# Performance work log

Hardware: AMD Instinct MI355X
Metric: run time of the kernel (lower is better)

## Reference

```python
import math
import jax, jax.numpy as jnp
import numpy as np

B = 4096
IN_FEATURES = 512
OUT_FEATURES = 1024
SPARSITY = 0.01  # kwta.sparsity
X_DENSITY = 0.1  # fraction of active bits in the binary SDR input


def setup_inputs() -> dict:
    key = jax.random.key(0)
    kx, kw = jax.random.split(key)
    # binary sparse SDR input (the module counts nonzeros, expects sparse binary x)
    x = (jax.random.uniform(kx, (B, IN_FEATURES)) < X_DENSITY).astype(jnp.float32)
    weight = jax.random.normal(kw, (OUT_FEATURES, IN_FEATURES), dtype=jnp.float32)
    return {"x": x, "weight": weight}


def reference(x, weight):
    Bn, in_f = x.shape
    out_f = weight.shape[0]
    k_active = math.ceil(SPARSITY * out_f)   # serial MP steps (11)
    k_in = math.ceil(SPARSITY * in_f)        # kwta winners on xr (6)
    rows = jnp.arange(Bn)

    nonzero = jnp.sum(x != 0, axis=1)
    lambd = (3 * jnp.max(nonzero) * in_f).astype(jnp.float32)

    def wta(r):  # one-hot argmax per row -> binary [B, out_f]
        idx = jnp.argmax(r, axis=1)
        return jnp.zeros_like(r).at[rows, idx].set(1.0)

    def kwta(v):  # binary top-k per row -> binary [B, in_f]
        _, idx = jax.lax.top_k(v, k_in)
        return jnp.zeros_like(v).at[rows[:, None], idx].set(1.0)

    two_x = 2.0 * x
    wT = weight.T  # [in_f, out_f]

    def step(carry, _):
        encoded, xr = carry
        residual = (two_x - xr) @ wT - lambd * encoded      # [B, out_f]
        encoded = encoded + wta(residual)
        xr = kwta(encoded @ weight)                          # [B, in_f]
        return (encoded, xr), None

    init = (jnp.zeros((Bn, out_f), jnp.float32), jnp.zeros_like(x))
    (encoded, xr), _ = jax.lax.scan(step, init, None, length=k_active)
    return encoded, xr
```

## Files before the change

kernel.cpp:

```cpp
#include <hip/hip_runtime.h>

#define IN_F 512
#define OUT_F 1024
#define K_ACTIVE 11
#define K_IN 6

__global__ __launch_bounds__(256) void transpose_w_kernel(const float* __restrict__ w,
                                                          float* __restrict__ wT) {
    __shared__ float tile[32][33];
    const int tx = threadIdx.x & 31;
    const int ty = threadIdx.x >> 5;
    const int i0 = blockIdx.x * 32;
    const int j0 = blockIdx.y * 32;
#pragma unroll
    for (int k = 0; k < 4; ++k)
        tile[ty + 8 * k][tx] = w[(size_t)(j0 + ty + 8 * k) * IN_F + (i0 + tx)];
    __syncthreads();
#pragma unroll
    for (int k = 0; k < 4; ++k)
        wT[(size_t)(i0 + ty + 8 * k) * OUT_F + (j0 + tx)] = tile[tx][ty + 8 * k];
}
__global__ void zero_row_f_kernel(float* __restrict__ wT) {
    wT[(size_t)IN_F * OUT_F + blockIdx.x * 256 + threadIdx.x] = 0.0f;
}

__device__ __forceinline__ unsigned long long pack_key(double v, unsigned rev,
                                                       unsigned long long mask) {
    unsigned long long b = (unsigned long long)__double_as_longlong(v);
    unsigned long long m =
        (unsigned long long)((long long)b >> 63) | 0x8000000000000000ull;
    unsigned long long u = b ^ m;
    return (u & ~mask) | (unsigned long long)rev;
}

__device__ __forceinline__ unsigned hi_key(double v) {
    const int hi = __double2hiint(v);
    return (unsigned)hi ^ ((unsigned)(hi >> 31) | 0x80000000u);
}

template <int C>
__device__ __forceinline__ unsigned maxdpp(unsigned v) {
    unsigned t = (unsigned)__builtin_amdgcn_update_dpp(0, (int)v, C, 0xF, 0xF, true);
    return t > v ? t : v;
}
__device__ __forceinline__ unsigned wave_umax(unsigned v) {
    v = maxdpp<0x111>(v);
    v = maxdpp<0x112>(v);
    v = maxdpp<0x114>(v);
    v = maxdpp<0x118>(v);
    v = maxdpp<0x142>(v);
    v = maxdpp<0x143>(v);
    return (unsigned)__builtin_amdgcn_readlane((int)v, 63);
}

__device__ __forceinline__ unsigned long long wave_max_key(unsigned long long k) {
    const unsigned h = (unsigned)(k >> 32), l = (unsigned)k;
    const unsigned gh = wave_umax(h);
    const unsigned long long tied = __ballot(h == gh);
    unsigned gl;
    if (__popcll(tied) == 1) {
        gl = (unsigned)__builtin_amdgcn_readlane((int)l,
                                                 (int)__ffsll((long long)tied) - 1);
    } else {
        gl = wave_umax((h == gh) ? l : 0u);
    }
    return ((unsigned long long)gh << 32) | gl;
}

__device__ __forceinline__ void half_add2(double* rh, const float* __restrict__ wT,
                                          int i0, int i1, int lane, int wv) {
    const float* p0 = wT + ((size_t)i0 << 10) + (wv << 9) + (lane << 2);
    const float* p1 = wT + ((size_t)i1 << 10) + (wv << 9) + (lane << 2);
    const float4 f0 = *(const float4*)(p0);
    const float4 f1 = *(const float4*)(p0 + 256);
    const float4 g0 = *(const float4*)(p1);
    const float4 g1 = *(const float4*)(p1 + 256);
    rh[0] += (double)f0.x + (double)g0.x;  rh[1] += (double)f0.y + (double)g0.y;
    rh[2] += (double)f0.z + (double)g0.z;  rh[3] += (double)f0.w + (double)g0.w;
    rh[4] += (double)f1.x + (double)g1.x;  rh[5] += (double)f1.y + (double)g1.y;
    rh[6] += (double)f1.z + (double)g1.z;  rh[7] += (double)f1.w + (double)g1.w;
}

__device__ __forceinline__ void half_axpy(double* rh, const float* __restrict__ wT,
                                          int i, double sgn, int lane, int wv) {
    const float* rp = wT + ((size_t)i << 10) + (wv << 9) + (lane << 2);
    const float4 f0 = *(const float4*)(rp);
    const float4 f1 = *(const float4*)(rp + 256);
    rh[0] += sgn * (double)f0.x;  rh[1] += sgn * (double)f0.y;
    rh[2] += sgn * (double)f0.z;  rh[3] += sgn * (double)f0.w;
    rh[4] += sgn * (double)f1.x;  rh[5] += sgn * (double)f1.y;
    rh[6] += sgn * (double)f1.z;  rh[7] += sgn * (double)f1.w;
}

__device__ __forceinline__ void half_add0(double* rh, const float* __restrict__ w,
                                          int i, int lane, int wv) {
#pragma unroll
    for (int s = 0; s < 8; ++s) {
        const int j = (wv << 9) | ((s >> 2) << 8) | (lane << 2) | (s & 3);
        rh[s] += (double)w[(size_t)j * IN_F + i];
    }
}
__device__ __forceinline__ void half_axpy0(double* rh, const float* __restrict__ w,
                                           int i, double sgn, int lane, int wv) {
#pragma unroll
    for (int s = 0; s < 8; ++s) {
        const int j = (wv << 9) | ((s >> 2) << 8) | (lane << 2) | (s & 3);
        rh[s] += sgn * (double)w[(size_t)j * IN_F + i];
    }
}

template <int MODE>
__global__ __launch_bounds__(128) void bmp_kernel(const float* __restrict__ x,
                                                  const float* __restrict__ w,
                                                  const float* __restrict__ wT,
                                                  float* __restrict__ out, int rows) {
    __shared__ unsigned short act[IN_F + 8];
    __shared__ unsigned gu32[2][2];
    __shared__ int gjw[2][2];
    __shared__ unsigned long long kx[2];
    const int lane = threadIdx.x & 63;
    const int wv = threadIdx.x >> 6;
    const int row = blockIdx.x;
    if (row >= rows) return;

    const float* xrow = x + (size_t)row * IN_F;
    int cnt = 0;
#pragma unroll
    for (int c = 0; c < IN_F / 64; ++c) {
        bool pbit = xrow[c * 64 + lane] != 0.0f;
        unsigned long long m = __ballot(pbit);
        int pre = __popcll(m & ((1ull << lane) - 1ull));
        if (wv == 0 && pbit) act[cnt + pre] = (unsigned short)(c * 64 + lane);
        cnt += __popcll(m);
    }
    if (wv == 0 && lane < 2) act[cnt + lane] = (unsigned short)IN_F;
    __syncthreads();

    double r[8];
#pragma unroll
    for (int s = 0; s < 8; ++s) r[s] = 0.0;
    if constexpr (MODE == 1) {
#pragma unroll 1
        for (int k = 0; k < cnt; k += 2) half_add2(r, wT, act[k], act[k + 1], lane, wv);
    } else {
#pragma unroll 1
        for (int k = 0; k < cnt; ++k) half_add0(r, w, act[k], lane, wv);
    }
#pragma unroll
    for (int s = 0; s < 8; ++s) r[s] *= 2.0;

    double vd[8];
#pragma unroll
    for (int p = 0; p < 8; ++p) vd[p] = 0.0;

    unsigned enc = 0;
    unsigned selmask = 0;
    int O0 = -1, O1 = -1, O2 = -1, O3 = -1, O4 = -1, O5 = -1;

#pragma unroll 1
    for (int t = 0; t < K_ACTIVE; ++t) {
        unsigned k8[8];
#pragma unroll
        for (int s = 0; s < 8; ++s) {
            const unsigned key = hi_key(r[s]);
            k8[s] = (enc & (1u << s)) ? 0u : key;
        }
        {
            unsigned lm = k8[0];
#pragma unroll
            for (int s = 1; s < 8; ++s) lm = k8[s] > lm ? k8[s] : lm;
            const unsigned g = wave_umax(lm);
            const unsigned long long tied = __ballot(lm == g);
            unsigned mm = 0;
#pragma unroll
            for (int s = 0; s < 8; ++s) mm |= (k8[s] == g) ? (1u << s) : 0u;
            const int L = (int)__ffsll((long long)tied) - 1;
            const unsigned mmL = (unsigned)__builtin_amdgcn_readlane((int)mm, L);
            int jw;
            if (__builtin_expect((__popcll(tied) == 1) && !(mmL & (mmL - 1)), 1)) {
                const int bi = __ffs(mmL) - 1;
                jw = (wv << 9) | ((bi >> 2) << 8) | (L << 2) | (bi & 3);
            } else {
                unsigned long long kb = 0;
#pragma unroll
                for (int s = 0; s < 8; ++s) {
                    const int j = (wv << 9) | ((s >> 2) << 8) | (lane << 2) | (s & 3);
                    const unsigned long long fk =
                        pack_key(r[s], 1023u ^ (unsigned)j, 1023ull);
                    kb = (k8[s] == g && fk > kb) ? fk : kb;
                }
                const unsigned long long gk = wave_max_key(kb);
                jw = 1023 ^ (int)(gk & 1023ull);
            }
            if (lane == 0) {
                gu32[t & 1][wv] = g;
                gjw[t & 1][wv] = jw;
            }
        }
        __syncthreads();
        const unsigned ga = gu32[t & 1][0], gb = gu32[t & 1][1];
        int bestj;
        if (__builtin_expect(ga != gb, 1)) {
            bestj = (gb > ga) ? gjw[t & 1][1] : gjw[t & 1][0];
        } else {
            unsigned long long kb = 0;
#pragma unroll
            for (int s = 0; s < 8; ++s) {
                const int j = (wv << 9) | ((s >> 2) << 8) | (lane << 2) | (s & 3);
                const unsigned long long fk =
                    pack_key(r[s], 1023u ^ (unsigned)j, 1023ull);
                kb = (k8[s] == ga && fk > kb) ? fk : kb;
            }
            const unsigned long long wm = wave_max_key(kb);
            if (lane == 0) kx[wv] = wm;
            __syncthreads();
            const unsigned long long A = kx[0], B = kx[1];
            bestj = 1023 ^ (int)((A > B ? A : B) & 1023ull);
        }
        bestj = __builtin_amdgcn_readfirstlane(bestj);
        if ((bestj >> 9) == wv && ((bestj >> 2) & 63) == lane)
            enc |= 1u << ((((bestj >> 8) & 1) << 2) | (bestj & 3));

        {
            const float* wr = w + ((size_t)bestj << 9) + (lane << 2);
            const float4 f0 = *(const float4*)wr;
            const float4 f1 = *(const float4*)(wr + 256);
            vd[0] += (double)f0.x;  vd[1] += (double)f0.y;
            vd[2] += (double)f0.z;  vd[3] += (double)f0.w;
            vd[4] += (double)f1.x;  vd[5] += (double)f1.y;
            vd[6] += (double)f1.z;  vd[7] += (double)f1.w;
        }

        int N0, N1, N2, N3, N4, N5;
        {
            unsigned kk[8];
#pragma unroll
            for (int p = 0; p < 8; ++p) kk[p] = hi_key(vd[p]);
            int N[6];
#pragma unroll
            for (int s2 = 0; s2 < K_IN; ++s2) {
                unsigned lm = kk[0];
#pragma unroll
                for (int p = 1; p < 8; ++p) lm = kk[p] > lm ? kk[p] : lm;
                const unsigned g2 = wave_umax(lm);
                const unsigned long long tied2 = __ballot(lm == g2);
                unsigned mm2 = 0;
#pragma unroll
                for (int p = 0; p < 8; ++p) mm2 |= (kk[p] == g2) ? (1u << p) : 0u;
                const int L2 = (int)__ffsll((long long)tied2) - 1;
                const unsigned mmL2 =
                    (unsigned)__builtin_amdgcn_readlane((int)mm2, L2);
                int n;
                if (__builtin_expect((__popcll(tied2) == 1) && !(mmL2 & (mmL2 - 1)),
                                     1)) {
                    const int bp = __ffs(mmL2) - 1;
                    n = ((bp >> 2) << 8) | (L2 << 2) | (bp & 3);
#pragma unroll
                    for (int p = 0; p < 8; ++p) kk[p] = (kk[p] == g2) ? 0u : kk[p];
                } else {
                    unsigned long long kb = 0;
#pragma unroll
                    for (int p = 0; p < 8; ++p) {
                        const int i = ((p >> 2) << 8) | (lane << 2) | (p & 3);
                        const unsigned long long fk =
                            pack_key(vd[p], 511u ^ (unsigned)i, 511ull);
                        kb = (kk[p] == g2 && fk > kb) ? fk : kb;
                    }
                    const unsigned long long gk = wave_max_key(kb);
                    n = 511 ^ (int)(gk & 511ull);
                    const int ln = (n >> 2) & 63;
                    const int bp = (((n >> 8) & 1) << 2) | (n & 3);
#pragma unroll
                    for (int p = 0; p < 8; ++p)
                        kk[p] = (lane == ln && p == bp) ? 0u : kk[p];
                }
                N[s2] = __builtin_amdgcn_readfirstlane(n);
            }
            if (t == K_ACTIVE - 1) {
                selmask = 0;
#pragma unroll
                for (int p = 0; p < 8; ++p) selmask |= (kk[p] == 0u) ? (1u << p) : 0u;
            }
            N0 = N[0]; N1 = N[1]; N2 = N[2]; N3 = N[3]; N4 = N[4]; N5 = N[5];
        }

        if (t == 0) {
            if constexpr (MODE == 1) {
                half_axpy(r, wT, N0, -1.0, lane, wv);
                half_axpy(r, wT, N1, -1.0, lane, wv);
                half_axpy(r, wT, N2, -1.0, lane, wv);
                half_axpy(r, wT, N3, -1.0, lane, wv);
                half_axpy(r, wT, N4, -1.0, lane, wv);
                half_axpy(r, wT, N5, -1.0, lane, wv);
            } else {
                half_axpy0(r, w, N0, -1.0, lane, wv);
                half_axpy0(r, w, N1, -1.0, lane, wv);
                half_axpy0(r, w, N2, -1.0, lane, wv);
                half_axpy0(r, w, N3, -1.0, lane, wv);
                half_axpy0(r, w, N4, -1.0, lane, wv);
                half_axpy0(r, w, N5, -1.0, lane, wv);
            }
        } else if (t < K_ACTIVE - 1) {
#pragma unroll
            for (int a2 = 0; a2 < 6; ++a2) {
                const int o = (a2 == 0) ? O0 : (a2 == 1) ? O1 : (a2 == 2) ? O2
                              : (a2 == 3) ? O3 : (a2 == 4) ? O4 : O5;
                const bool stay = (o == N0) | (o == N1) | (o == N2) |
                                  (o == N3) | (o == N4) | (o == N5);
                if (!stay) {
                    if constexpr (MODE == 1) half_axpy(r, wT, o, 1.0, lane, wv);
                    else half_axpy0(r, w, o, 1.0, lane, wv);
                }
            }
#pragma unroll
            for (int b2 = 0; b2 < 6; ++b2) {
                const int n = (b2 == 0) ? N0 : (b2 == 1) ? N1 : (b2 == 2) ? N2
                              : (b2 == 3) ? N3 : (b2 == 4) ? N4 : N5;
                const bool was = (n == O0) | (n == O1) | (n == O2) |
                                 (n == O3) | (n == O4) | (n == O5);
                if (!was) {
                    if constexpr (MODE == 1) half_axpy(r, wT, n, -1.0, lane, wv);
                    else half_axpy0(r, w, n, -1.0, lane, wv);
                }
            }
        }
        O0 = N0; O1 = N1; O2 = N2; O3 = N3; O4 = N4; O5 = N5;
    }

    float* oe = out + (size_t)row * OUT_F + (wv << 9) + (lane << 2);
#pragma unroll
    for (int c = 0; c < 2; ++c) {
        float4 v;
        v.x = (enc & (1u << (4 * c + 0))) ? 1.0f : 0.0f;
        v.y = (enc & (1u << (4 * c + 1))) ? 1.0f : 0.0f;
        v.z = (enc & (1u << (4 * c + 2))) ? 1.0f : 0.0f;
        v.w = (enc & (1u << (4 * c + 3))) ? 1.0f : 0.0f;
        *(float4*)(oe + (c << 8)) = v;
    }
    if (wv == 0) {
        float* ox = out + (size_t)rows * OUT_F + (size_t)row * IN_F + (lane << 2);
#pragma unroll
        for (int c = 0; c < 2; ++c) {
            float4 v;
            v.x = (selmask & (1u << (4 * c + 0))) ? 1.0f : 0.0f;
            v.y = (selmask & (1u << (4 * c + 1))) ? 1.0f : 0.0f;
            v.z = (selmask & (1u << (4 * c + 2))) ? 1.0f : 0.0f;
            v.w = (selmask & (1u << (4 * c + 3))) ? 1.0f : 0.0f;
            *(float4*)(ox + (c << 8)) = v;
        }
    }
}

extern "C" void kernel_launch(void* const* d_in, const int* in_sizes, int n_in,
                              void* d_out, int out_size, void* d_ws, size_t ws_size,
                              hipStream_t stream) {
    const float* x = (const float*)d_in[0];
    const float* w = (const float*)d_in[1];
    float* out = (float*)d_out;
    const int rows = in_sizes[0] / IN_F;

    const size_t need_f = (size_t)(IN_F + 1) * OUT_F * sizeof(float);

    if (d_ws != nullptr && ws_size >= need_f) {
        float* wT = (float*)d_ws;
        transpose_w_kernel<<<dim3(IN_F / 32, OUT_F / 32), 256, 0, stream>>>(w, wT);
        zero_row_f_kernel<<<OUT_F / 256, 256, 0, stream>>>(wT);
        bmp_kernel<1><<<rows, 128, 0, stream>>>(x, w, wT, out, rows);
    } else {
        bmp_kernel<0><<<rows, 128, 0, stream>>>(x, w, nullptr, out, rows);
    }
}
```

Measured before the change: 156.2 us.

## Process two rows per block, splitting the kWTA stage across waves

Result: slower. 196.5 us (+25.8%).

```diff
diff --git a/kernel.cpp b/kernel.cpp
--- a/kernel.cpp
+++ b/kernel.cpp
@@ -110,98 +110,91 @@
 }
 
 template <int MODE>
-__global__ __launch_bounds__(128) void bmp_kernel(const float* __restrict__ x,
-                                                  const float* __restrict__ w,
-                                                  const float* __restrict__ wT,
-                                                  float* __restrict__ out, int rows) {
-    __shared__ unsigned short act[IN_F + 8];
+__global__ __launch_bounds__(128, 4) void bmp_kernel(const float* __restrict__ x,
+                                                     const float* __restrict__ w,
+                                                     const float* __restrict__ wT,
+                                                     float* __restrict__ out,
+                                                     int rows) {
+    __shared__ unsigned short act[2][IN_F + 8];
+    __shared__ int cntS[2];
     __shared__ unsigned gu32[2][2];
     __shared__ int gjw[2][2];
-    __shared__ unsigned long long kx[2];
+    __shared__ unsigned long long kx[2][2];
+    __shared__ int msg[2][8];
     const int lane = threadIdx.x & 63;
     const int wv = threadIdx.x >> 6;
-    const int row = blockIdx.x;
-    if (row >= rows) return;
-
-    const float* xrow = x + (size_t)row * IN_F;
-    int cnt = 0;
-#pragma unroll
-    for (int c = 0; c < IN_F / 64; ++c) {
-        bool pbit = xrow[c * 64 + lane] != 0.0f;
-        unsigned long long m = __ballot(pbit);
-        int pre = __popcll(m & ((1ull << lane) - 1ull));
-        if (wv == 0 && pbit) act[cnt + pre] = (unsigned short)(c * 64 + lane);
-        cnt += __popcll(m);
-    }
-    if (wv == 0 && lane < 2) act[cnt + lane] = (unsigned short)IN_F;
+    const int rowA = blockIdx.x * 2;
+    if (rowA >= rows) return;
+    int rowB = rowA + 1;
+    if (rowB >= rows) rowB = rowA;
+    const int myrow = wv ? rowB : rowA;
+
+    {
+        const float* xrow = x + (size_t)myrow * IN_F;
+        int cnt = 0;
+#pragma unroll
+        for (int c = 0; c < IN_F / 64; ++c) {
+            bool pbit = xrow[c * 64 + lane] != 0.0f;
+            unsigned long long m = __ballot(pbit);
+            int pre = __popcll(m & ((1ull << lane) - 1ull));
+            if (pbit) act[wv][cnt + pre] = (unsigned short)(c * 64 + lane);
+            cnt += __popcll(m);
+        }
+        if (lane < 2) act[wv][cnt + lane] = (unsigned short)IN_F;
+        if (lane == 0) cntS[wv] = cnt;
+    }
     __syncthreads();
-
-    double r[8];
-#pragma unroll
-    for (int s = 0; s < 8; ++s) r[s] = 0.0;
+    const int cntA = cntS[0], cntB = cntS[1];
+
+    double rA[8], rB[8];
+#pragma unroll
+    for (int s = 0; s < 8; ++s) { rA[s] = 0.0; rB[s] = 0.0; }
     if constexpr (MODE == 1) {
 #pragma unroll 1
-        for (int k = 0; k < cnt; k += 2) half_add2(r, wT, act[k], act[k + 1], lane, wv);
+        for (int k = 0; k < cntA; k += 2)
+            half_add2(rA, wT, act[0][k], act[0][k + 1], lane, wv);
+#pragma unroll 1
+        for (int k = 0; k < cntB; k += 2)
+            half_add2(rB, wT, act[1][k], act[1][k + 1], lane, wv);
     } else {
 #pragma unroll 1
-        for (int k = 0; k < cnt; ++k) half_add0(r, w, act[k], lane, wv);
-    }
-#pragma unroll
-    for (int s = 0; s < 8; ++s) r[s] *= 2.0;
+        for (int k = 0; k < cntA; ++k) half_add0(rA, w, act[0][k], lane, wv);
+#pragma unroll 1
+        for (int k = 0; k < cntB; ++k) half_add0(rB, w, act[1][k], lane, wv);
+    }
+#pragma unroll
+    for (int s = 0; s < 8; ++s) { rA[s] *= 2.0; rB[s] *= 2.0; }
 
     double vd[8];
 #pragma unroll
     for (int p = 0; p < 8; ++p) vd[p] = 0.0;
 
-    unsigned enc = 0;
+    unsigned encA = 0, encB = 0;
     unsigned selmask = 0;
-    int O0 = -1, O1 = -1, O2 = -1, O3 = -1, O4 = -1, O5 = -1;
-
-#pragma unroll 1
-    for (int t = 0; t < K_ACTIVE; ++t) {
+    int OA0 = -1, OA1 = -1, OA2 = -1, OA3 = -1, OA4 = -1, OA5 = -1;
+    int OB0 = -1, OB1 = -1, OB2 = -1, OB3 = -1, OB4 = -1, OB5 = -1;
+
+    auto amax_half = [&](const double* r, unsigned enc, int rsel) {
         unsigned k8[8];
 #pragma unroll
         for (int s = 0; s < 8; ++s) {
             const unsigned key = hi_key(r[s]);
             k8[s] = (enc & (1u << s)) ? 0u : key;
         }
-        {
-            unsigned lm = k8[0];
-#pragma unroll
-            for (int s = 1; s < 8; ++s) lm = k8[s] > lm ? k8[s] : lm;
-            const unsigned g = wave_umax(lm);
-            const unsigned long long tied = __ballot(lm == g);
-            unsigned mm = 0;
-#pragma unroll
-            for (int s = 0; s < 8; ++s) mm |= (k8[s] == g) ? (1u << s) : 0u;
-            const int L = (int)__ffsll((long long)tied) - 1;
-            const unsigned mmL = (unsigned)__builtin_amdgcn_readlane((int)mm, L);
-            int jw;
-            if (__builtin_expect((__popcll(tied) == 1) && !(mmL & (mmL - 1)), 1)) {
-                const int bi = __ffs(mmL) - 1;
-                jw = (wv << 9) | ((bi >> 2) << 8) | (L << 2) | (bi & 3);
-            } else {
-                unsigned long long kb = 0;
-#pragma unroll
-                for (int s = 0; s < 8; ++s) {
-                    const int j = (wv << 9) | ((s >> 2) << 8) | (lane << 2) | (s & 3);
-                    const unsigned long long fk =
-                        pack_key(r[s], 1023u ^ (unsigned)j, 1023ull);
-                    kb = (k8[s] == g && fk > kb) ? fk : kb;
-                }
-                const unsigned long long gk = wave_max_key(kb);
-                jw = 1023 ^ (int)(gk & 1023ull);
-            }
-            if (lane == 0) {
-                gu32[t & 1][wv] = g;
-                gjw[t & 1][wv] = jw;
-            }
-        }
-        __syncthreads();
-        const unsigned ga = gu32[t & 1][0], gb = gu32[t & 1][1];
-        int bestj;
-        if (__builtin_expect(ga != gb, 1)) {
-            bestj = (gb > ga) ? gjw[t & 1][1] : gjw[t & 1][0];
+        unsigned lm = k8[0];
+#pragma unroll
+        for (int s = 1; s < 8; ++s) lm = k8[s] > lm ? k8[s] : lm;
+        const unsigned g = wave_umax(lm);
+        const unsigned long long tied = __ballot(lm == g);
+        unsigned mm = 0;
+#pragma unroll
+        for (int s = 0; s < 8; ++s) mm |= (k8[s] == g) ? (1u << s) : 0u;
+        const int L = (int)__ffsll((long long)tied) - 1;
+        const unsigned mmL = (unsigned)__builtin_amdgcn_readlane((int)mm, L);
+        int jw;
+        if (__builtin_expect((__popcll(tied) == 1) && !(mmL & (mmL - 1)), 1)) {
+            const int bi = __ffs(mmL) - 1;
+            jw = (wv << 9) | ((bi >> 2) << 8) | (L << 2) | (bi & 3);
         } else {
             unsigned long long kb = 0;
 #pragma unroll
@@ -209,34 +202,66 @@
                 const int j = (wv << 9) | ((s >> 2) << 8) | (lane << 2) | (s & 3);
                 const unsigned long long fk =
                     pack_key(r[s], 1023u ^ (unsigned)j, 1023ull);
-                kb = (k8[s] == ga && fk > kb) ? fk : kb;
+                kb = (k8[s] == g && fk > kb) ? fk : kb;
+            }
+            const unsigned long long gk = wave_max_key(kb);
+            jw = 1023 ^ (int)(gk & 1023ull);
+        }
+        if (lane == 0) {
+            gu32[rsel][wv] = g;
+            gjw[rsel][wv] = jw;
+        }
+    };
+
+    auto merge_row = [&](int rsel, const double* r, unsigned enc) -> int {
+        const unsigned ga = gu32[rsel][0], gb = gu32[rsel][1];
+        int bestj;
+        if (__builtin_expect(ga != gb, 1)) {
+            bestj = (gb > ga) ? gjw[rsel][1] : gjw[rsel][0];
+        } else {
+            unsigned long long kb = 0;
+#pragma unroll
+            for (int s = 0; s < 8; ++s) {
+                const int j = (wv << 9) | ((s >> 2) << 8) | (lane << 2) | (s & 3);
+                const unsigned long long fk =
+                    pack_key(r[s], 1023u ^ (unsigned)j, 1023ull);
+                const bool cand = !(enc & (1u << s)) && hi_key(r[s]) == ga;
+                kb = (cand && fk > kb) ? fk : kb;
             }
             const unsigned long long wm = wave_max_key(kb);
-            if (lane == 0) kx[wv] = wm;
+            if (lane == 0) kx[rsel][wv] = wm;
             __syncthreads();
-            const unsigned long long A = kx[0], B = kx[1];
+            const unsigned long long A = kx[rsel][0], B = kx[rsel][1];
             bestj = 1023 ^ (int)((A > B ? A : B) & 1023ull);
         }
-        bestj = __builtin_amdgcn_readfirstlane(bestj);
-        if ((bestj >> 9) == wv && ((bestj >> 2) & 63) == lane)
-            enc |= 1u << ((((bestj >> 8) & 1) << 2) | (bestj & 3));
+        return __builtin_amdgcn_readfirstlane(bestj);
+    };
+
+#pragma unroll 1
+    for (int t = 0; t < K_ACTIVE; ++t) {
+        amax_half(rA, encA, 0);
+        amax_half(rB, encB, 1);
+        __syncthreads();
+        const int bestjA = merge_row(0, rA, encA);
+        const int bestjB = merge_row(1, rB, encB);
+        if ((bestjA >> 9) == wv && ((bestjA >> 2) & 63) == lane)
+            encA |= 1u << ((((bestjA >> 8) & 1) << 2) | (bestjA & 3));
+        if ((bestjB >> 9) == wv && ((bestjB >> 2) & 63) == lane)
+            encB |= 1u << ((((bestjB >> 8) & 1) << 2) | (bestjB & 3));
 
         {
-            const float* wr = w + ((size_t)bestj << 9) + (lane << 2);
+            const int bj = wv ? bestjB : bestjA;
+            const float* wr = w + ((size_t)bj << 9) + (lane << 2);
             const float4 f0 = *(const float4*)wr;
             const float4 f1 = *(const float4*)(wr + 256);
             vd[0] += (double)f0.x;  vd[1] += (double)f0.y;
             vd[2] += (double)f0.z;  vd[3] += (double)f0.w;
             vd[4] += (double)f1.x;  vd[5] += (double)f1.y;
             vd[6] += (double)f1.z;  vd[7] += (double)f1.w;
-        }
-
-        int N0, N1, N2, N3, N4, N5;
-        {
+
             unsigned kk[8];
 #pragma unroll
             for (int p = 0; p < 8; ++p) kk[p] = hi_key(vd[p]);
-            int N[6];
 #pragma unroll
             for (int s2 = 0; s2 < K_IN; ++s2) {
                 unsigned lm = kk[0];
@@ -274,71 +299,137 @@
                     for (int p = 0; p < 8; ++p)
                         kk[p] = (lane == ln && p == bp) ? 0u : kk[p];
                 }
-                N[s2] = __builtin_amdgcn_readfirstlane(n);
+                if (lane == 0) msg[wv][1 + s2] = n;
             }
             if (t == K_ACTIVE - 1) {
                 selmask = 0;
 #pragma unroll
                 for (int p = 0; p < 8; ++p) selmask |= (kk[p] == 0u) ? (1u << p) : 0u;
             }
-            N0 = N[0]; N1 = N[1]; N2 = N[2]; N3 = N[3]; N4 = N[4]; N5 = N[5];
-        }
-
-        if (t == 0) {
-            if constexpr (MODE == 1) {
-                half_axpy(r, wT, N0, -1.0, lane, wv);
-                half_axpy(r, wT, N1, -1.0, lane, wv);
-                half_axpy(r, wT, N2, -1.0, lane, wv);
-                half_axpy(r, wT, N3, -1.0, lane, wv);
-                half_axpy(r, wT, N4, -1.0, lane, wv);
-                half_axpy(r, wT, N5, -1.0, lane, wv);
+        }
+        __syncthreads();
+
+        if (t < K_ACTIVE - 1) {
+            const int NA0 = __builtin_amdgcn_readfirstlane(msg[0][1]);
+            const int NA1 = __builtin_amdgcn_readfirstlane(msg[0][2]);
+            const int NA2 = __builtin_amdgcn_readfirstlane(msg[0][3]);
+            const int NA3 = __builtin_amdgcn_readfirstlane(msg[0][4]);
+            const int NA4 = __builtin_amdgcn_readfirstlane(msg[0][5]);
+            const int NA5 = __builtin_amdgcn_readfirstlane(msg[0][6]);
+            const int NB0 = __builtin_amdgcn_readfirstlane(msg[1][1]);
+            const int NB1 = __builtin_amdgcn_readfirstlane(msg[1][2]);
+            const int NB2 = __builtin_amdgcn_readfirstlane(msg[1][3]);
+            const int NB3 = __builtin_amdgcn_readfirstlane(msg[1][4]);
+            const int NB4 = __builtin_amdgcn_readfirstlane(msg[1][5]);
+            const int NB5 = __builtin_amdgcn_readfirstlane(msg[1][6]);
+
+            if (t == 0) {
+                if constexpr (MODE == 1) {
+                    half_axpy(rA, wT, NA0, -1.0, lane, wv);
+                    half_axpy(rA, wT, NA1, -1.0, lane, wv);
+                    half_axpy(rA, wT, NA2, -1.0, lane, wv);
+                    half_axpy(rA, wT, NA3, -1.0, lane, wv);
+                    half_axpy(rA, wT, NA4, -1.0, lane, wv);
+                    half_axpy(rA, wT, NA5, -1.0, lane, wv);
+                } else {
+                    half_axpy0(rA, w, NA0, -1.0, lane, wv);
+                    half_axpy0(rA, w, NA1, -1.0, lane, wv);
+                    half_axpy0(rA, w, NA2, -1.0, lane, wv);
+                    half_axpy0(rA, w, NA3, -1.0, lane, wv);
+                    half_axpy0(rA, w, NA4, -1.0, lane, wv);
+                    half_axpy0(rA, w, NA5, -1.0, lane, wv);
+                }
             } else {
-                half_axpy0(r, w, N0, -1.0, lane, wv);
-                half_axpy0(r, w, N1, -1.0, lane, wv);
-                half_axpy0(r, w, N2, -1.0, lane, wv);
-                half_axpy0(r, w, N3, -1.0, lane, wv);
-                half_axpy0(r, w, N4, -1.0, lane, wv);
-                half_axpy0(r, w, N5, -1.0, lane, wv);
-            }
-        } else if (t < K_ACTIVE - 1) {
-#pragma unroll
-            for (int a2 = 0; a2 < 6; ++a2) {
-                const int o = (a2 == 0) ? O0 : (a2 == 1) ? O1 : (a2 == 2) ? O2
-                              : (a2 == 3) ? O3 : (a2 == 4) ? O4 : O5;
-                const bool stay = (o == N0) | (o == N1) | (o == N2) |
-                                  (o == N3) | (o == N4) | (o == N5);
-                if (!stay) {
-                    if constexpr (MODE == 1) half_axpy(r, wT, o, 1.0, lane, wv);
-                    else half_axpy0(r, w, o, 1.0, lane, wv);
-                }
-            }
-#pragma unroll
-            for (int b2 = 0; b2 < 6; ++b2) {
-                const int n = (b2 == 0) ? N0 : (b2 == 1) ? N1 : (b2 == 2) ? N2
-                              : (b2 == 3) ? N3 : (b2 == 4) ? N4 : N5;
-                const bool was = (n == O0) | (n == O1) | (n == O2) |
-                                 (n == O3) | (n == O4) | (n == O5);
-                if (!was) {
-                    if constexpr (MODE == 1) half_axpy(r, wT, n, -1.0, lane, wv);
-                    else half_axpy0(r, w, n, -1.0, lane, wv);
-                }
-            }
-        }
-        O0 = N0; O1 = N1; O2 = N2; O3 = N3; O4 = N4; O5 = N5;
-    }
-
-    float* oe = out + (size_t)row * OUT_F + (wv << 9) + (lane << 2);
-#pragma unroll
-    for (int c = 0; c < 2; ++c) {
-        float4 v;
-        v.x = (enc & (1u << (4 * c + 0))) ? 1.0f : 0.0f;
-        v.y = (enc & (1u << (4 * c + 1))) ? 1.0f : 0.0f;
-        v.z = (enc & (1u << (4 * c + 2))) ? 1.0f : 0.0f;
-        v.w = (enc & (1u << (4 * c + 3))) ? 1.0f : 0.0f;
-        *(float4*)(oe + (c << 8)) = v;
-    }
-    if (wv == 0) {
-        float* ox = out + (size_t)rows * OUT_F + (size_t)row * IN_F + (lane << 2);
+#pragma unroll
+                for (int a2 = 0; a2 < 6; ++a2) {
+                    const int o = (a2 == 0) ? OA0 : (a2 == 1) ? OA1 : (a2 == 2) ? OA2
+                                  : (a2 == 3) ? OA3 : (a2 == 4) ? OA4 : OA5;
+                    const bool stay = (o == NA0) | (o == NA1) | (o == NA2) |
+                                      (o == NA3) | (o == NA4) | (o == NA5);
+                    if (!stay) {
+                        if constexpr (MODE == 1) half_axpy(rA, wT, o, 1.0, lane, wv);
+                        else half_axpy0(rA, w, o, 1.0, lane, wv);
+                    }
+                }
+#pragma unroll
+                for (int b2 = 0; b2 < 6; ++b2) {
+                    const int n = (b2 == 0) ? NA0 : (b2 == 1) ? NA1 : (b2 == 2) ? NA2
+                                  : (b2 == 3) ? NA3 : (b2 == 4) ? NA4 : NA5;
+                    const bool was = (n == OA0) | (n == OA1) | (n == OA2) |
+                                     (n == OA3) | (n == OA4) | (n == OA5);
+                    if (!was) {
+                        if constexpr (MODE == 1) half_axpy(rA, wT, n, -1.0, lane, wv);
+                        else half_axpy0(rA, w, n, -1.0, lane, wv);
+                    }
+                }
+            }
+            if (t == 0) {
+                if constexpr (MODE == 1) {
+                    half_axpy(rB, wT, NB0, -1.0, lane, wv);
+                    half_axpy(rB, wT, NB1, -1.0, lane, wv);
+                    half_axpy(rB, wT, NB2, -1.0, lane, wv);
+                    half_axpy(rB, wT, NB3, -1.0, lane, wv);
+                    half_axpy(rB, wT, NB4, -1.0, lane, wv);
+                    half_axpy(rB, wT, NB5, -1.0, lane, wv);
+                } else {
+                    half_axpy0(rB, w, NB0, -1.0, lane, wv);
+                    half_axpy0(rB, w, NB1, -1.0, lane, wv);
+                    half_axpy0(rB, w, NB2, -1.0, lane, wv);
+                    half_axpy0(rB, w, NB3, -1.0, lane, wv);
+                    half_axpy0(rB, w, NB4, -1.0, lane, wv);
+                    half_axpy0(rB, w, NB5, -1.0, lane, wv);
+                }
+            } else {
+#pragma unroll
+                for (int a2 = 0; a2 < 6; ++a2) {
+                    const int o = (a2 == 0) ? OB0 : (a2 == 1) ? OB1 : (a2 == 2) ? OB2
+                                  : (a2 == 3) ? OB3 : (a2 == 4) ? OB4 : OB5;
+                    const bool stay = (o == NB0) | (o == NB1) | (o == NB2) |
+                                      (o == NB3) | (o == NB4) | (o == NB5);
+                    if (!stay) {
+                        if constexpr (MODE == 1) half_axpy(rB, wT, o, 1.0, lane, wv);
+                        else half_axpy0(rB, w, o, 1.0, lane, wv);
+                    }
+                }
+#pragma unroll
+                for (int b2 = 0; b2 < 6; ++b2) {
+                    const int n = (b2 == 0) ? NB0 : (b2 == 1) ? NB1 : (b2 == 2) ? NB2
+                                  : (b2 == 3) ? NB3 : (b2 == 4) ? NB4 : NB5;
+                    const bool was = (n == OB0) | (n == OB1) | (n == OB2) |
+                                     (n == OB3) | (n == OB4) | (n == OB5);
+                    if (!was) {
+                        if constexpr (MODE == 1) half_axpy(rB, wT, n, -1.0, lane, wv);
+                        else half_axpy0(rB, w, n, -1.0, lane, wv);
+                    }
+                }
+            }
+            OA0 = NA0; OA1 = NA1; OA2 = NA2; OA3 = NA3; OA4 = NA4; OA5 = NA5;
+            OB0 = NB0; OB1 = NB1; OB2 = NB2; OB3 = NB3; OB4 = NB4; OB5 = NB5;
+        }
+    }
+
+    {
+        float* oeA = out + (size_t)rowA * OUT_F + (wv << 9) + (lane << 2);
+#pragma unroll
+        for (int c = 0; c < 2; ++c) {
+            float4 v;
+            v.x = (encA & (1u << (4 * c + 0))) ? 1.0f : 0.0f;
+            v.y = (encA & (1u << (4 * c + 1))) ? 1.0f : 0.0f;
+            v.z = (encA & (1u << (4 * c + 2))) ? 1.0f : 0.0f;
+            v.w = (encA & (1u << (4 * c + 3))) ? 1.0f : 0.0f;
+            *(float4*)(oeA + (c << 8)) = v;
+        }
+        float* oeB = out + (size_t)rowB * OUT_F + (wv << 9) + (lane << 2);
+#pragma unroll
+        for (int c = 0; c < 2; ++c) {
+            float4 v;
+            v.x = (encB & (1u << (4 * c + 0))) ? 1.0f : 0.0f;
+            v.y = (encB & (1u << (4 * c + 1))) ? 1.0f : 0.0f;
+            v.z = (encB & (1u << (4 * c + 2))) ? 1.0f : 0.0f;
+            v.w = (encB & (1u << (4 * c + 3))) ? 1.0f : 0.0f;
+            *(float4*)(oeB + (c << 8)) = v;
+        }
+        float* ox = out + (size_t)rows * OUT_F + (size_t)myrow * IN_F + (lane << 2);
 #pragma unroll
         for (int c = 0; c < 2; ++c) {
             float4 v;
@@ -360,13 +451,14 @@
     const int rows = in_sizes[0] / IN_F;
 
     const size_t need_f = (size_t)(IN_F + 1) * OUT_F * sizeof(float);
+    const int blocks = (rows + 1) / 2;
 
     if (d_ws != nullptr && ws_size >= need_f) {
         float* wT = (float*)d_ws;
         transpose_w_kernel<<<dim3(IN_F / 32, OUT_F / 32), 256, 0, stream>>>(w, wT);
         zero_row_f_kernel<<<OUT_F / 256, 256, 0, stream>>>(wT);
-        bmp_kernel<1><<<rows, 128, 0, stream>>>(x, w, wT, out, rows);
+        bmp_kernel<1><<<blocks, 128, 0, stream>>>(x, w, wT, out, rows);
     } else {
-        bmp_kernel<0><<<rows, 128, 0, stream>>>(x, w, nullptr, out, rows);
-    }
-}
+        bmp_kernel<0><<<blocks, 128, 0, stream>>>(x, w, nullptr, out, rows);
+    }
+}
```

## Compute kWTA on one wave, share axpy list via LDS, prefetch weight rows

Applied to the files above, without the earlier changes.

New measurement: 152.3 us. -2.5%, faster.

```diff
diff --git a/kernel.cpp b/kernel.cpp
--- a/kernel.cpp
+++ b/kernel.cpp
@@ -67,31 +67,6 @@
     return ((unsigned long long)gh << 32) | gl;
 }
 
-__device__ __forceinline__ void half_add2(double* rh, const float* __restrict__ wT,
-                                          int i0, int i1, int lane, int wv) {
-    const float* p0 = wT + ((size_t)i0 << 10) + (wv << 9) + (lane << 2);
-    const float* p1 = wT + ((size_t)i1 << 10) + (wv << 9) + (lane << 2);
-    const float4 f0 = *(const float4*)(p0);
-    const float4 f1 = *(const float4*)(p0 + 256);
-    const float4 g0 = *(const float4*)(p1);
-    const float4 g1 = *(const float4*)(p1 + 256);
-    rh[0] += (double)f0.x + (double)g0.x;  rh[1] += (double)f0.y + (double)g0.y;
-    rh[2] += (double)f0.z + (double)g0.z;  rh[3] += (double)f0.w + (double)g0.w;
-    rh[4] += (double)f1.x + (double)g1.x;  rh[5] += (double)f1.y + (double)g1.y;
-    rh[6] += (double)f1.z + (double)g1.z;  rh[7] += (double)f1.w + (double)g1.w;
-}
-
-__device__ __forceinline__ void half_axpy(double* rh, const float* __restrict__ wT,
-                                          int i, double sgn, int lane, int wv) {
-    const float* rp = wT + ((size_t)i << 10) + (wv << 9) + (lane << 2);
-    const float4 f0 = *(const float4*)(rp);
-    const float4 f1 = *(const float4*)(rp + 256);
-    rh[0] += sgn * (double)f0.x;  rh[1] += sgn * (double)f0.y;
-    rh[2] += sgn * (double)f0.z;  rh[3] += sgn * (double)f0.w;
-    rh[4] += sgn * (double)f1.x;  rh[5] += sgn * (double)f1.y;
-    rh[6] += sgn * (double)f1.z;  rh[7] += sgn * (double)f1.w;
-}
-
 __device__ __forceinline__ void half_add0(double* rh, const float* __restrict__ w,
                                           int i, int lane, int wv) {
 #pragma unroll
@@ -118,6 +93,8 @@
     __shared__ unsigned gu32[2][2];
     __shared__ int gjw[2][2];
     __shared__ unsigned long long kx[2];
+    __shared__ int axlist[16];
+    __shared__ int axn;
     const int lane = threadIdx.x & 63;
     const int wv = threadIdx.x >> 6;
     const int row = blockIdx.x;
@@ -140,8 +117,26 @@
 #pragma unroll
     for (int s = 0; s < 8; ++s) r[s] = 0.0;
     if constexpr (MODE == 1) {
-#pragma unroll 1
-        for (int k = 0; k < cnt; k += 2) half_add2(r, wT, act[k], act[k + 1], lane, wv);
+        const int base = (wv << 9) + (lane << 2);
+        const float* pa = wT + ((size_t)act[0] << 10) + base;
+        const float* pb = wT + ((size_t)act[1] << 10) + base;
+        float4 c0 = *(const float4*)pa, c1 = *(const float4*)(pa + 256);
+        float4 c2 = *(const float4*)pb, c3 = *(const float4*)(pb + 256);
+#pragma unroll 1
+        for (int k = 0; k < cnt; k += 2) {
+            float4 n0 = c0, n1 = c1, n2 = c2, n3 = c3;
+            if (k + 2 < cnt) {
+                const float* qa = wT + ((size_t)act[k + 2] << 10) + base;
+                const float* qb = wT + ((size_t)act[k + 3] << 10) + base;
+                n0 = *(const float4*)qa;  n1 = *(const float4*)(qa + 256);
+                n2 = *(const float4*)qb;  n3 = *(const float4*)(qb + 256);
+            }
+            r[0] += (double)c0.x + (double)c2.x;  r[1] += (double)c0.y + (double)c2.y;
+            r[2] += (double)c0.z + (double)c2.z;  r[3] += (double)c0.w + (double)c2.w;
+            r[4] += (double)c1.x + (double)c3.x;  r[5] += (double)c1.y + (double)c3.y;
+            r[6] += (double)c1.z + (double)c3.z;  r[7] += (double)c1.w + (double)c3.w;
+            c0 = n0; c1 = n1; c2 = n2; c3 = n3;
+        }
     } else {
 #pragma unroll 1
         for (int k = 0; k < cnt; ++k) half_add0(r, w, act[k], lane, wv);
@@ -221,7 +216,7 @@
         if ((bestj >> 9) == wv && ((bestj >> 2) & 63) == lane)
             enc |= 1u << ((((bestj >> 8) & 1) << 2) | (bestj & 3));
 
-        {
+        if (wv == 0) {
             const float* wr = w + ((size_t)bestj << 9) + (lane << 2);
             const float4 f0 = *(const float4*)wr;
             const float4 f1 = *(const float4*)(wr + 256);
@@ -229,14 +224,11 @@
             vd[2] += (double)f0.z;  vd[3] += (double)f0.w;
             vd[4] += (double)f1.x;  vd[5] += (double)f1.y;
             vd[6] += (double)f1.z;  vd[7] += (double)f1.w;
-        }
-
-        int N0, N1, N2, N3, N4, N5;
-        {
+
+            int N[6];
             unsigned kk[8];
 #pragma unroll
             for (int p = 0; p < 8; ++p) kk[p] = hi_key(vd[p]);
-            int N[6];
 #pragma unroll
             for (int s2 = 0; s2 < K_IN; ++s2) {
                 unsigned lm = kk[0];
@@ -281,50 +273,73 @@
 #pragma unroll
                 for (int p = 0; p < 8; ++p) selmask |= (kk[p] == 0u) ? (1u << p) : 0u;
             }
-            N0 = N[0]; N1 = N[1]; N2 = N[2]; N3 = N[3]; N4 = N[4]; N5 = N[5];
-        }
-
-        if (t == 0) {
+
+            if (lane == 0) {
+                int n2 = 0;
+                if (t == 0) {
+#pragma unroll
+                    for (int b = 0; b < 6; ++b) axlist[n2++] = ~N[b];
+                } else if (t < K_ACTIVE - 1) {
+#pragma unroll
+                    for (int a2 = 0; a2 < 6; ++a2) {
+                        const int o = (a2 == 0) ? O0 : (a2 == 1) ? O1 : (a2 == 2) ? O2
+                                      : (a2 == 3) ? O3 : (a2 == 4) ? O4 : O5;
+                        const bool stay = (o == N[0]) | (o == N[1]) | (o == N[2]) |
+                                          (o == N[3]) | (o == N[4]) | (o == N[5]);
+                        if (!stay) axlist[n2++] = o;
+                    }
+#pragma unroll
+                    for (int b = 0; b < 6; ++b) {
+                        const int nn = N[b];
+                        const bool was = (nn == O0) | (nn == O1) | (nn == O2) |
+                                         (nn == O3) | (nn == O4) | (nn == O5);
+                        if (!was) axlist[n2++] = ~nn;
+                    }
+                }
+                axn = n2;
+            }
+            O0 = N[0]; O1 = N[1]; O2 = N[2]; O3 = N[3]; O4 = N[4]; O5 = N[5];
+        }
+        __syncthreads();
+
+        const int nax = axn;
+        if (nax > 0) {
             if constexpr (MODE == 1) {
-                half_axpy(r, wT, N0, -1.0, lane, wv);
-                half_axpy(r, wT, N1, -1.0, lane, wv);
-                half_axpy(r, wT, N2, -1.0, lane, wv);
-                half_axpy(r, wT, N3, -1.0, lane, wv);
-                half_axpy(r, wT, N4, -1.0, lane, wv);
-                half_axpy(r, wT, N5, -1.0, lane, wv);
+                const int base = (wv << 9) + (lane << 2);
+                int e0 = axlist[0];
+                {
+                    const int i0 = (e0 < 0) ? ~e0 : e0;
+                    const float* p = wT + ((size_t)i0 << 10) + base;
+                    float4 A0 = *(const float4*)p;
+                    float4 A1 = *(const float4*)(p + 256);
+#pragma unroll 1
+                    for (int k = 0; k < nax; ++k) {
+                        float4 B0 = A0, B1 = A1;
+                        int e1 = 0;
+                        if (k + 1 < nax) {
+                            e1 = axlist[k + 1];
+                            const int i1 = (e1 < 0) ? ~e1 : e1;
+                            const float* q = wT + ((size_t)i1 << 10) + base;
+                            B0 = *(const float4*)q;
+                            B1 = *(const float4*)(q + 256);
+                        }
+                        const double sg = (e0 < 0) ? -1.0 : 1.0;
+                        r[0] += sg * (double)A0.x;  r[1] += sg * (double)A0.y;
+                        r[2] += sg * (double)A0.z;  r[3] += sg * (double)A0.w;
+                        r[4] += sg * (double)A1.x;  r[5] += sg * (double)A1.y;
+                        r[6] += sg * (double)A1.z;  r[7] += sg * (double)A1.w;
+                        A0 = B0; A1 = B1; e0 = e1;
+                    }
+                }
             } else {
-                half_axpy0(r, w, N0, -1.0, lane, wv);
-                half_axpy0(r, w, N1, -1.0, lane, wv);
-                half_axpy0(r, w, N2, -1.0, lane, wv);
-                half_axpy0(r, w, N3, -1.0, lane, wv);
-                half_axpy0(r, w, N4, -1.0, lane, wv);
-                half_axpy0(r, w, N5, -1.0, lane, wv);
-            }
-        } else if (t < K_ACTIVE - 1) {
-#pragma unroll
-            for (int a2 = 0; a2 < 6; ++a2) {
-                const int o = (a2 == 0) ? O0 : (a2 == 1) ? O1 : (a2 == 2) ? O2
-                              : (a2 == 3) ? O3 : (a2 == 4) ? O4 : O5;
-                const bool stay = (o == N0) | (o == N1) | (o == N2) |
-                                  (o == N3) | (o == N4) | (o == N5);
-                if (!stay) {
-                    if constexpr (MODE == 1) half_axpy(r, wT, o, 1.0, lane, wv);
-                    else half_axpy0(r, w, o, 1.0, lane, wv);
-                }
-            }
-#pragma unroll
-            for (int b2 = 0; b2 < 6; ++b2) {
-                const int n = (b2 == 0) ? N0 : (b2 == 1) ? N1 : (b2 == 2) ? N2
-                              : (b2 == 3) ? N3 : (b2 == 4) ? N4 : N5;
-                const bool was = (n == O0) | (n == O1) | (n == O2) |
-                                 (n == O3) | (n == O4) | (n == O5);
-                if (!was) {
-                    if constexpr (MODE == 1) half_axpy(r, wT, n, -1.0, lane, wv);
-                    else half_axpy0(r, w, n, -1.0, lane, wv);
-                }
-            }
-        }
-        O0 = N0; O1 = N1; O2 = N2; O3 = N3; O4 = N4; O5 = N5;
+#pragma unroll 1
+                for (int k = 0; k < nax; ++k) {
+                    const int e = axlist[k];
+                    const int i = (e < 0) ? ~e : e;
+                    half_axpy0(r, w, i, (e < 0) ? -1.0 : 1.0, lane, wv);
+                }
+            }
+        }
     }
 
     float* oe = out + (size_t)row * OUT_F + (wv << 9) + (lane << 2);
```
